# Optimization experiments

Measured on AMD Instinct MI355X. Metric: run time of the kernel, lower is better.

Reference implementation:

```python
import jax, jax.numpy as jnp
import numpy as np

HIDDEN = 1024
HEADS = 16
HEAD_DIM = HIDDEN // HEADS
SCALE = 1.0 / float(np.sqrt(HEAD_DIM))


def setup_inputs() -> dict:
    key = jax.random.key(0)
    k1, k2, k3, k4 = jax.random.split(key, 4)
    B, N, C = 4, 2048, HIDDEN
    x = jax.random.normal(k1, (B, N, C), dtype=jnp.float32)
    # nn.Linear(C, 3C, bias=False): y = x @ W_qkv where W_qkv is [C, 3C]
    w_qkv = jax.random.normal(k2, (C, 3 * C), dtype=jnp.float32) * (1.0 / np.sqrt(C))
    # nn.Linear(C, C) with bias
    w_out = jax.random.normal(k3, (C, C), dtype=jnp.float32) * (1.0 / np.sqrt(C))
    b_out = jax.random.normal(k4, (C,), dtype=jnp.float32) * 0.01
    return {"x": x, "w_qkv": w_qkv, "w_out": w_out, "b_out": b_out}


def reference(x, w_qkv, w_out, b_out):
    B, N, C = x.shape
    H, D = HEADS, HEAD_DIM
    qkv = jnp.einsum("bnc,cf->bnf", x, w_qkv)  # [B, N, 3C]
    qkv = qkv.reshape(B, N, 3, H, D).transpose(2, 0, 3, 1, 4)  # [3, B, H, N, D]
    q, k, v = qkv[0], qkv[1], qkv[2]
    attn = jnp.einsum("bhnd,bhmd->bhnm", q, k) * SCALE  # [B, H, N, N]
    attn = jax.nn.softmax(attn, axis=-1)
    # dropout is identity in eval mode
    out = jnp.einsum("bhnm,bhmd->bhnd", attn, v)  # [B, H, N, D]
    out = out.transpose(0, 2, 1, 3).reshape(B, N, C)
    return jnp.einsum("bnc,co->bno", out, w_out) + b_out
```

## Files before the change

### kernel.cpp

```cpp
#include <hip/hip_runtime.h>
#include <hip/hip_bf16.h>
#include <stdint.h>

#define SEQ   2048
#define NBH   64
#define DH    64
#define CH    1024
#define MTOT  8192
#define QSCALE 0.1803368801111204f

typedef __bf16 bf16_t;
typedef bf16_t bf16x8 __attribute__((ext_vector_type(8)));
typedef float  f32x4  __attribute__((ext_vector_type(4)));
typedef float  f32x16 __attribute__((ext_vector_type(16)));

__device__ __forceinline__ bf16_t to_bf16(float f) {
  uint32_t u = __builtin_bit_cast(uint32_t, f);
  uint16_t r = (uint16_t)((u + 0x7fffu + ((u >> 16) & 1u)) >> 16);
  return __builtin_bit_cast(bf16_t, r);
}

__device__ __forceinline__ void gload_lds16(const void* g, void* l) {
  __builtin_amdgcn_global_load_lds(
      (const __attribute__((address_space(1))) uint32_t*)g,
      (__attribute__((address_space(3))) uint32_t*)l, 16, 0, 0);
}

__device__ __forceinline__ f32x4 mfma_bf16(bf16x8 a, bf16x8 b, f32x4 c) {
  return __builtin_amdgcn_mfma_f32_16x16x32_bf16(a, b, c, 0, 0, 0);
}
__device__ __forceinline__ f32x16 mfma32_bf16(bf16x8 a, bf16x8 b, f32x16 c) {
  return __builtin_amdgcn_mfma_f32_32x32x16_bf16(a, b, c, 0, 0, 0);
}

__device__ __forceinline__ float exp2_fast(float x) {
#if __has_builtin(__builtin_amdgcn_exp2f)
  return __builtin_amdgcn_exp2f(x);
#else
  float r;
  asm("v_exp_f32 %0, %1\ns_nop 0" : "=v"(r) : "v"(x));
  return r;
#endif
}

__device__ __forceinline__ uint32_t cvt_pk_bf16(float lo, float hi) {
  uint32_t r;
  asm("v_cvt_pk_bf16_f32 %0, %1, %2" : "=v"(r) : "v"(lo), "v"(hi));
  return r;
}

__device__ __forceinline__ void permlane32_swap(uint32_t& a, uint32_t& b) {
  asm("s_nop 1\n\tv_permlane32_swap_b32 %0, %1\n\ts_nop 1" : "+v"(a), "+v"(b));
}


__global__ void cvt_f32_bf16(const float* __restrict__ in, bf16_t* __restrict__ out, int n) {
  int i = (blockIdx.x * 256 + threadIdx.x) * 4;
  const int stride = gridDim.x * 256 * 4;
  for (; i < n; i += stride) {
    const float4 f = *reinterpret_cast<const float4*>(in + i);
    bf16_t tmp[4] = {to_bf16(f.x), to_bf16(f.y), to_bf16(f.z), to_bf16(f.w)};
    *reinterpret_cast<uint2*>(out + i) = *reinterpret_cast<uint2*>(tmp);
  }
}

__global__ __launch_bounds__(256) void transpose_cvt(
    const float* __restrict__ W, bf16_t* __restrict__ WT, int Kd, int Nd) {
  __shared__ float t[64 * 65];
  const int n0 = blockIdx.x * 64, k0 = blockIdx.y * 64;
  const int tid = threadIdx.x;
#pragma unroll
  for (int rr = 0; rr < 16; ++rr) {
    const int idx = rr * 256 + tid;
    const int r = idx >> 6, c = idx & 63;
    t[r * 65 + c] = W[(size_t)(k0 + r) * Nd + n0 + c];
  }
  __syncthreads();
#pragma unroll
  for (int rr = 0; rr < 16; ++rr) {
    const int idx = rr * 256 + tid;
    const int nr = idx >> 6, kc = idx & 63;
    WT[(size_t)(n0 + nr) * Kd + k0 + kc] = to_bf16(t[kc * 65 + nr]);
  }
}


template <int EPI>
__global__ __launch_bounds__(256, 3) void gemm_bt(
    const bf16_t* __restrict__ A, const bf16_t* __restrict__ BT, int K, int nx,
    bf16_t* __restrict__ qb, bf16_t* __restrict__ kb, bf16_t* __restrict__ vb,
    const float* __restrict__ bias, float* __restrict__ out) {
  __shared__ __attribute__((aligned(16))) bf16_t lA[128 * 64];
  __shared__ __attribute__((aligned(16))) bf16_t lB[128 * 64];
  const int tid = threadIdx.x;
  const int lane = tid & 63;
  const int wv = tid >> 6;
  const int wm = wv >> 1, wn = wv & 1;

  const int nwg = gridDim.x;
  int bid = blockIdx.x;
  bid = (bid & 7) * (nwg >> 3) + (bid >> 3);
  const int m0 = (bid / nx) * 128, n0 = (bid % nx) * 128;

  const int l15 = lane & 15, l16 = lane >> 4;

  f32x4 acc[4][4] = {};

  const int srow = tid >> 3;
  const int sch = tid & 7;

  for (int kt = 0; kt < K; kt += 64) {
#pragma unroll
    for (int c = 0; c < 4; ++c) {
      const int row = c * 32 + srow;
      const int cs = sch ^ (row & 7);
      gload_lds16(A + (size_t)(m0 + row) * K + kt + cs * 8, &lA[c * 2048 + tid * 8]);
    }
#pragma unroll
    for (int c = 0; c < 4; ++c) {
      const int row = c * 32 + srow;
      const int cs = sch ^ (row & 7);
      gload_lds16(BT + (size_t)(n0 + row) * K + kt + cs * 8, &lB[c * 2048 + tid * 8]);
    }
    __syncthreads();
#pragma unroll
    for (int ks = 0; ks < 2; ++ks) {
      bf16x8 af[4], bfr[4];
#pragma unroll
      for (int i = 0; i < 4; ++i) {
        const int ar = wm * 64 + i * 16 + l15;
        const int cha = (ks * 4 + l16) ^ (ar & 7);
        af[i] = *reinterpret_cast<const bf16x8*>(&lA[ar * 64 + cha * 8]);
        const int br = wn * 64 + i * 16 + l15;
        const int chb = (ks * 4 + l16) ^ (br & 7);
        bfr[i] = *reinterpret_cast<const bf16x8*>(&lB[br * 64 + chb * 8]);
      }
#pragma unroll
      for (int i = 0; i < 4; ++i)
#pragma unroll
        for (int j = 0; j < 4; ++j)
          acc[i][j] = mfma_bf16(af[i], bfr[j], acc[i][j]);
    }
    __syncthreads();
  }

  if (EPI == 0) {
    const int f0 = n0 + wn * 64;
    const int three = f0 >> 10;
#pragma unroll
    for (int i = 0; i < 4; ++i) {
#pragma unroll
      for (int j = 0; j < 4; ++j) {
#pragma unroll
        for (int r = 0; r < 4; ++r) {
          const int m = m0 + wm * 64 + i * 16 + l16 * 4 + r;
          const int f = f0 + j * 16 + l15;
          const int h = (f >> 6) & 15, d = f & 63;
          const int bh = (m >> 11) * 16 + h;
          const int n = m & 2047;
          const float val = acc[i][j][r];
          if (three == 0)
            qb[((size_t)bh * SEQ + n) * DH + d] = to_bf16(val * QSCALE);
          else if (three == 1)
            kb[((size_t)bh * SEQ + n) * DH + d] = to_bf16(val);
          else
            vb[((size_t)bh * DH + d) * SEQ + n] = to_bf16(val);
        }
      }
    }
  } else {
#pragma unroll
    for (int j = 0; j < 4; ++j) {
      const int cc = n0 + wn * 64 + j * 16 + l15;
      const float bb = bias[cc];
#pragma unroll
      for (int i = 0; i < 4; ++i) {
#pragma unroll
        for (int r = 0; r < 4; ++r) {
          const int m = m0 + wm * 64 + i * 16 + l16 * 4 + r;
          out[(size_t)m * CH + cc] = acc[i][j][r] + bb;
        }
      }
    }
  }
}

__global__ __launch_bounds__(256, 4) void attn_fwd(
    const bf16_t* __restrict__ Q, const bf16_t* __restrict__ K,
    const bf16_t* __restrict__ V, bf16_t* __restrict__ O) {
  __shared__ __attribute__((aligned(16))) bf16_t lK[2][64 * 64];
  __shared__ __attribute__((aligned(16))) bf16_t lV[2][64 * 64];
  const int tid = threadIdx.x;
  const int lane = tid & 63;
  const int wv = tid >> 6;
  const int l31 = lane & 31, hi = lane >> 5;

  const int lin = blockIdx.x;
  const int bh = (lin & 7) * 8 + ((lin >> 3) & 7);
  const int qb = lin >> 6;
  const int q0w = qb * 128 + wv * 32;

  const bf16_t* Qb = Q + (size_t)bh * SEQ * DH;
  const bf16_t* Kb = K + (size_t)bh * SEQ * DH;
  const bf16_t* Vb = V + (size_t)bh * DH * SEQ;

  bf16x8 qf[4];
#pragma unroll
  for (int ks = 0; ks < 4; ++ks)
    qf[ks] = *reinterpret_cast<const bf16x8*>(
        Qb + (size_t)(q0w + l31) * DH + ks * 16 + hi * 8);

  f32x16 o0 = {}, o1 = {};
  float rs = 0.f;

  const int srow = tid >> 3;
  const int sch = tid & 7;

  auto stage = [&](int buf, int kt0) {
#pragma unroll
    for (int c = 0; c < 2; ++c) {
      const int row = c * 32 + srow;
      const int cs = sch ^ (row & 7);
      gload_lds16(Kb + (size_t)(kt0 + row) * DH + cs * 8, &lK[buf][c * 2048 + tid * 8]);
      gload_lds16(Vb + (size_t)row * SEQ + kt0 + cs * 8, &lV[buf][c * 2048 + tid * 8]);
    }
  };

  stage(0, 0);
  __syncthreads();
  int cur = 0;

  for (int t = 0; t < SEQ / 64; ++t) {
    if (t + 1 < SEQ / 64) stage(cur ^ 1, (t + 1) * 64);

    f32x16 s0 = {}, s1 = {};
    __builtin_amdgcn_s_setprio(1);
#pragma unroll
    for (int ks = 0; ks < 4; ++ks) {
      {
        const int row = l31;
        const int ch = (ks * 2 + hi) ^ (row & 7);
        const bf16x8 kf = *reinterpret_cast<const bf16x8*>(&lK[cur][row * 64 + ch * 8]);
        s0 = mfma32_bf16(kf, qf[ks], s0);
      }
      {
        const int row = 32 + l31;
        const int ch = (ks * 2 + hi) ^ (row & 7);
        const bf16x8 kf = *reinterpret_cast<const bf16x8*>(&lK[cur][row * 64 + ch * 8]);
        s1 = mfma32_bf16(kf, qf[ks], s1);
      }
    }
    __builtin_amdgcn_s_setprio(0);

#pragma unroll
    for (int j = 0; j < 16; ++j) { s0[j] = exp2_fast(s0[j]); rs += s0[j]; }
#pragma unroll
    for (int j = 0; j < 16; ++j) { s1[j] = exp2_fast(s1[j]); rs += s1[j]; }

    bf16x8 pa[4];
    {
      uint32_t a0 = cvt_pk_bf16(s0[0], s0[1]),   b0 = cvt_pk_bf16(s0[4], s0[5]);
      uint32_t a1 = cvt_pk_bf16(s0[2], s0[3]),   b1 = cvt_pk_bf16(s0[6], s0[7]);
      uint32_t a2 = cvt_pk_bf16(s0[8], s0[9]),   b2 = cvt_pk_bf16(s0[12], s0[13]);
      uint32_t a3 = cvt_pk_bf16(s0[10], s0[11]), b3 = cvt_pk_bf16(s0[14], s0[15]);
      permlane32_swap(a0, b0);
      permlane32_swap(a1, b1);
      permlane32_swap(a2, b2);
      permlane32_swap(a3, b3);
      union { uint32_t u[4]; bf16x8 v; } ua, ub, uc, ud;
      ua.u[0] = a0; ua.u[1] = a1; ua.u[2] = b0; ua.u[3] = b1; pa[0] = ua.v;
      ub.u[0] = a2; ub.u[1] = a3; ub.u[2] = b2; ub.u[3] = b3; pa[1] = ub.v;
      uint32_t c0 = cvt_pk_bf16(s1[0], s1[1]),   d0 = cvt_pk_bf16(s1[4], s1[5]);
      uint32_t c1 = cvt_pk_bf16(s1[2], s1[3]),   d1 = cvt_pk_bf16(s1[6], s1[7]);
      uint32_t c2 = cvt_pk_bf16(s1[8], s1[9]),   d2 = cvt_pk_bf16(s1[12], s1[13]);
      uint32_t c3 = cvt_pk_bf16(s1[10], s1[11]), d3 = cvt_pk_bf16(s1[14], s1[15]);
      permlane32_swap(c0, d0);
      permlane32_swap(c1, d1);
      permlane32_swap(c2, d2);
      permlane32_swap(c3, d3);
      uc.u[0] = c0; uc.u[1] = c1; uc.u[2] = d0; uc.u[3] = d1; pa[2] = uc.v;
      ud.u[0] = c2; ud.u[1] = c3; ud.u[2] = d2; ud.u[3] = d3; pa[3] = ud.v;
    }

    __builtin_amdgcn_s_setprio(1);
#pragma unroll
    for (int tt = 0; tt < 4; ++tt) {
      {
        const int row = l31;
        const int ch = (tt * 2 + hi) ^ (row & 7);
        const bf16x8 vf = *reinterpret_cast<const bf16x8*>(&lV[cur][row * 64 + ch * 8]);
        o0 = mfma32_bf16(pa[tt], vf, o0);
      }
      {
        const int row = 32 + l31;
        const int ch = (tt * 2 + hi) ^ (row & 7);
        const bf16x8 vf = *reinterpret_cast<const bf16x8*>(&lV[cur][row * 64 + ch * 8]);
        o1 = mfma32_bf16(pa[tt], vf, o1);
      }
    }
    __builtin_amdgcn_s_setprio(0);

    __syncthreads();
    cur ^= 1;
  }

  uint32_t ra = __builtin_bit_cast(uint32_t, rs), rb2 = ra;
  permlane32_swap(ra, rb2);
  const float tot = __builtin_bit_cast(float, ra) + __builtin_bit_cast(float, rb2);
  const float rinv = 1.0f / tot;

  const int b = bh >> 4, h = bh & 15;
#pragma unroll
  for (int r = 0; r < 16; ++r) {
    const int qr = (r & 3) + 8 * (r >> 2) + 4 * hi;
    const float inv = __shfl(rinv, qr, 64);
    const size_t grow = (size_t)(b * SEQ + q0w + qr) * CH + h * DH;
    O[grow + l31]      = to_bf16(o0[r] * inv);
    O[grow + 32 + l31] = to_bf16(o1[r] * inv);
  }
}


extern "C" void kernel_launch(void* const* d_in, const int* in_sizes, int n_in,
                              void* d_out, int out_size, void* d_ws, size_t ws_size,
                              hipStream_t stream) {
  const float* x     = (const float*)d_in[0];
  const float* w_qkv = (const float*)d_in[1];
  const float* w_out = (const float*)d_in[2];
  const float* b_out = (const float*)d_in[3];
  float* out = (float*)d_out;

  char* ws = (char*)d_ws;
  bf16_t* xb    = (bf16_t*)(ws);
  bf16_t* wqkvT = (bf16_t*)(ws + 16777216);
  bf16_t* woT   = (bf16_t*)(ws + 23068672);
  bf16_t* Qb    = (bf16_t*)(ws + 25165824);
  bf16_t* Kb    = (bf16_t*)(ws + 41943040);
  bf16_t* Vb    = (bf16_t*)(ws + 58720256);
  bf16_t* Ab    = xb;

  cvt_f32_bf16<<<2048, 256, 0, stream>>>(x, xb, MTOT * CH);
  transpose_cvt<<<dim3(3 * CH / 64, CH / 64), 256, 0, stream>>>(w_qkv, wqkvT, CH, 3 * CH);
  transpose_cvt<<<dim3(CH / 64, CH / 64), 256, 0, stream>>>(w_out, woT, CH, CH);

  gemm_bt<0><<<(3 * CH / 128) * (MTOT / 128), 256, 0, stream>>>(
      xb, wqkvT, CH, 3 * CH / 128, Qb, Kb, Vb, nullptr, nullptr);

  attn_fwd<<<1024, 256, 0, stream>>>(Qb, Kb, Vb, Ab);

  gemm_bt<1><<<(CH / 128) * (MTOT / 128), 256, 0, stream>>>(
      Ab, woT, CH, CH / 128, nullptr, nullptr, nullptr, b_out, out);
}
```

Baseline: 187.3 us.

## Compute softmax row sums via MFMA with ones, restructure attention tile loop

Replaces the per-thread VALU accumulation of softmax row sums with an extra MFMA against a ones vector, so the denominators come out in the same layout as the output accumulators and no cross-lane shuffle is needed at the end. The attention loop is unrolled by two with fixed LDS buffer offsets and precomputed swizzled read addresses. The exp/pack of the second half is interleaved with the PV MFMAs of the first half. The V epilogue in the QKV GEMM now writes packed 4-element bf16 vectors instead of scalar stores. This adds MFMA work (bf16-rounded P in the sum) in exchange for fewer VALU adds and less address arithmetic.

```diff
diff --git a/kernel.cpp b/kernel.cpp
--- a/kernel.cpp
+++ b/kernel.cpp
@@ -147,24 +147,39 @@
   if (EPI == 0) {
     const int f0 = n0 + wn * 64;
     const int three = f0 >> 10;
-#pragma unroll
-    for (int i = 0; i < 4; ++i) {
-#pragma unroll
-      for (int j = 0; j < 4; ++j) {
-#pragma unroll
-        for (int r = 0; r < 4; ++r) {
-          const int m = m0 + wm * 64 + i * 16 + l16 * 4 + r;
+    if (three < 2) {
+#pragma unroll
+      for (int i = 0; i < 4; ++i) {
+#pragma unroll
+        for (int j = 0; j < 4; ++j) {
+#pragma unroll
+          for (int r = 0; r < 4; ++r) {
+            const int m = m0 + wm * 64 + i * 16 + l16 * 4 + r;
+            const int f = f0 + j * 16 + l15;
+            const int h = (f >> 6) & 15, d = f & 63;
+            const int bh = (m >> 11) * 16 + h;
+            const int n = m & 2047;
+            const float val = acc[i][j][r];
+            if (three == 0)
+              qb[((size_t)bh * SEQ + n) * DH + d] = to_bf16(val * QSCALE);
+            else
+              kb[((size_t)bh * SEQ + n) * DH + d] = to_bf16(val);
+          }
+        }
+      }
+    } else {
+#pragma unroll
+      for (int i = 0; i < 4; ++i) {
+#pragma unroll
+        for (int j = 0; j < 4; ++j) {
+          const int m = m0 + wm * 64 + i * 16 + l16 * 4;
           const int f = f0 + j * 16 + l15;
           const int h = (f >> 6) & 15, d = f & 63;
           const int bh = (m >> 11) * 16 + h;
           const int n = m & 2047;
-          const float val = acc[i][j][r];
-          if (three == 0)
-            qb[((size_t)bh * SEQ + n) * DH + d] = to_bf16(val * QSCALE);
-          else if (three == 1)
-            kb[((size_t)bh * SEQ + n) * DH + d] = to_bf16(val);
-          else
-            vb[((size_t)bh * DH + d) * SEQ + n] = to_bf16(val);
+          const uint2 pk = make_uint2(cvt_pk_bf16(acc[i][j][0], acc[i][j][1]),
+                                      cvt_pk_bf16(acc[i][j][2], acc[i][j][3]));
+          *reinterpret_cast<uint2*>(&vb[((size_t)bh * DH + d) * SEQ + n]) = pk;
         }
       }
     }
@@ -188,8 +203,7 @@
 __global__ __launch_bounds__(256, 4) void attn_fwd(
     const bf16_t* __restrict__ Q, const bf16_t* __restrict__ K,
     const bf16_t* __restrict__ V, bf16_t* __restrict__ O) {
-  __shared__ __attribute__((aligned(16))) bf16_t lK[2][64 * 64];
-  __shared__ __attribute__((aligned(16))) bf16_t lV[2][64 * 64];
+  __shared__ __attribute__((aligned(16))) char lds[32768];
   const int tid = threadIdx.x;
   const int lane = tid & 63;
   const int wv = tid >> 6;
@@ -210,8 +224,21 @@
     qf[ks] = *reinterpret_cast<const bf16x8*>(
         Qb + (size_t)(q0w + l31) * DH + ks * 16 + hi * 8);
 
+  bf16x8 ones;
+#pragma unroll
+  for (int j = 0; j < 8; ++j) ones[j] = __builtin_bit_cast(bf16_t, (uint16_t)0x3F80);
+
   f32x16 o0 = {}, o1 = {};
-  float rs = 0.f;
+  f32x16 osum = {};
+
+  uint32_t raddr[2][4];
+#pragma unroll
+  for (int h = 0; h < 2; ++h) {
+    const int row = h * 32 + l31;
+#pragma unroll
+    for (int j = 0; j < 4; ++j)
+      raddr[h][j] = row * 128 + ((((j * 2 + hi) ^ (row & 7))) << 4);
+  }
 
   const int srow = tid >> 3;
   const int sch = tid & 7;
@@ -221,99 +248,98 @@
     for (int c = 0; c < 2; ++c) {
       const int row = c * 32 + srow;
       const int cs = sch ^ (row & 7);
-      gload_lds16(Kb + (size_t)(kt0 + row) * DH + cs * 8, &lK[buf][c * 2048 + tid * 8]);
-      gload_lds16(Vb + (size_t)row * SEQ + kt0 + cs * 8, &lV[buf][c * 2048 + tid * 8]);
+      gload_lds16(Kb + (size_t)(kt0 + row) * DH + cs * 8,
+                  lds + buf * 16384 + c * 4096 + tid * 16);
+      gload_lds16(Vb + (size_t)row * SEQ + kt0 + cs * 8,
+                  lds + buf * 16384 + 8192 + c * 4096 + tid * 16);
     }
   };
+
+#define ATT_TILE(KOFF, VOFF)                                                   \
+  {                                                                            \
+    f32x16 s0 = {}, s1 = {};                                                   \
+    __builtin_amdgcn_s_setprio(1);                                             \
+    _Pragma("unroll") for (int j = 0; j < 4; ++j) {                            \
+      const bf16x8 kf0 = *reinterpret_cast<const bf16x8*>(lds + raddr[0][j] + (KOFF)); \
+      s0 = mfma32_bf16(kf0, qf[j], s0);                                        \
+      const bf16x8 kf1 = *reinterpret_cast<const bf16x8*>(lds + raddr[1][j] + (KOFF)); \
+      s1 = mfma32_bf16(kf1, qf[j], s1);                                        \
+    }                                                                          \
+    __builtin_amdgcn_s_setprio(0);                                             \
+    _Pragma("unroll") for (int j = 0; j < 16; ++j) s0[j] = exp2_fast(s0[j]);   \
+    bf16x8 pa0, pa1;                                                           \
+    {                                                                          \
+      uint32_t a0 = cvt_pk_bf16(s0[0], s0[1]),   b0 = cvt_pk_bf16(s0[4], s0[5]);   \
+      uint32_t a1 = cvt_pk_bf16(s0[2], s0[3]),   b1 = cvt_pk_bf16(s0[6], s0[7]);   \
+      uint32_t a2 = cvt_pk_bf16(s0[8], s0[9]),   b2 = cvt_pk_bf16(s0[12], s0[13]); \
+      uint32_t a3 = cvt_pk_bf16(s0[10], s0[11]), b3 = cvt_pk_bf16(s0[14], s0[15]); \
+      permlane32_swap(a0, b0); permlane32_swap(a1, b1);                        \
+      permlane32_swap(a2, b2); permlane32_swap(a3, b3);                        \
+      union { uint32_t u[4]; bf16x8 v; } ua, ub;                               \
+      ua.u[0] = a0; ua.u[1] = a1; ua.u[2] = b0; ua.u[3] = b1; pa0 = ua.v;      \
+      ub.u[0] = a2; ub.u[1] = a3; ub.u[2] = b2; ub.u[3] = b3; pa1 = ub.v;      \
+    }                                                                          \
+    __builtin_amdgcn_s_setprio(1);                                             \
+    {                                                                          \
+      const bf16x8 vf00 = *reinterpret_cast<const bf16x8*>(lds + raddr[0][0] + (VOFF)); \
+      o0 = mfma32_bf16(pa0, vf00, o0);                                         \
+      const bf16x8 vf01 = *reinterpret_cast<const bf16x8*>(lds + raddr[1][0] + (VOFF)); \
+      o1 = mfma32_bf16(pa0, vf01, o1);                                         \
+      osum = mfma32_bf16(pa0, ones, osum);                                     \
+      const bf16x8 vf10 = *reinterpret_cast<const bf16x8*>(lds + raddr[0][1] + (VOFF)); \
+      o0 = mfma32_bf16(pa1, vf10, o0);                                         \
+      const bf16x8 vf11 = *reinterpret_cast<const bf16x8*>(lds + raddr[1][1] + (VOFF)); \
+      o1 = mfma32_bf16(pa1, vf11, o1);                                         \
+      osum = mfma32_bf16(pa1, ones, osum);                                     \
+    }                                                                          \
+    __builtin_amdgcn_s_setprio(0);                                             \
+    _Pragma("unroll") for (int j = 0; j < 16; ++j) s1[j] = exp2_fast(s1[j]);   \
+    bf16x8 pa2, pa3;                                                           \
+    {                                                                          \
+      uint32_t c0 = cvt_pk_bf16(s1[0], s1[1]),   d0 = cvt_pk_bf16(s1[4], s1[5]);   \
+      uint32_t c1 = cvt_pk_bf16(s1[2], s1[3]),   d1 = cvt_pk_bf16(s1[6], s1[7]);   \
+      uint32_t c2 = cvt_pk_bf16(s1[8], s1[9]),   d2 = cvt_pk_bf16(s1[12], s1[13]); \
+      uint32_t c3 = cvt_pk_bf16(s1[10], s1[11]), d3 = cvt_pk_bf16(s1[14], s1[15]); \
+      permlane32_swap(c0, d0); permlane32_swap(c1, d1);                        \
+      permlane32_swap(c2, d2); permlane32_swap(c3, d3);                        \
+      union { uint32_t u[4]; bf16x8 v; } uc, ud;                               \
+      uc.u[0] = c0; uc.u[1] = c1; uc.u[2] = d0; uc.u[3] = d1; pa2 = uc.v;      \
+      ud.u[0] = c2; ud.u[1] = c3; ud.u[2] = d2; ud.u[3] = d3; pa3 = ud.v;      \
+    }                                                                          \
+    __builtin_amdgcn_s_setprio(1);                                             \
+    {                                                                          \
+      const bf16x8 vf20 = *reinterpret_cast<const bf16x8*>(lds + raddr[0][2] + (VOFF)); \
+      o0 = mfma32_bf16(pa2, vf20, o0);                                         \
+      const bf16x8 vf21 = *reinterpret_cast<const bf16x8*>(lds + raddr[1][2] + (VOFF)); \
+      o1 = mfma32_bf16(pa2, vf21, o1);                                         \
+      osum = mfma32_bf16(pa2, ones, osum);                                     \
+      const bf16x8 vf30 = *reinterpret_cast<const bf16x8*>(lds + raddr[0][3] + (VOFF)); \
+      o0 = mfma32_bf16(pa3, vf30, o0);                                         \
+      const bf16x8 vf31 = *reinterpret_cast<const bf16x8*>(lds + raddr[1][3] + (VOFF)); \
+      o1 = mfma32_bf16(pa3, vf31, o1);                                         \
+      osum = mfma32_bf16(pa3, ones, osum);                                     \
+    }                                                                          \
+    __builtin_amdgcn_s_setprio(0);                                             \
+  }
 
   stage(0, 0);
   __syncthreads();
-  int cur = 0;
-
-  for (int t = 0; t < SEQ / 64; ++t) {
-    if (t + 1 < SEQ / 64) stage(cur ^ 1, (t + 1) * 64);
-
-    f32x16 s0 = {}, s1 = {};
-    __builtin_amdgcn_s_setprio(1);
-#pragma unroll
-    for (int ks = 0; ks < 4; ++ks) {
-      {
-        const int row = l31;
-        const int ch = (ks * 2 + hi) ^ (row & 7);
-        const bf16x8 kf = *reinterpret_cast<const bf16x8*>(&lK[cur][row * 64 + ch * 8]);
-        s0 = mfma32_bf16(kf, qf[ks], s0);
-      }
-      {
-        const int row = 32 + l31;
-        const int ch = (ks * 2 + hi) ^ (row & 7);
-        const bf16x8 kf = *reinterpret_cast<const bf16x8*>(&lK[cur][row * 64 + ch * 8]);
-        s1 = mfma32_bf16(kf, qf[ks], s1);
-      }
-    }
-    __builtin_amdgcn_s_setprio(0);
-
-#pragma unroll
-    for (int j = 0; j < 16; ++j) { s0[j] = exp2_fast(s0[j]); rs += s0[j]; }
-#pragma unroll
-    for (int j = 0; j < 16; ++j) { s1[j] = exp2_fast(s1[j]); rs += s1[j]; }
-
-    bf16x8 pa[4];
-    {
-      uint32_t a0 = cvt_pk_bf16(s0[0], s0[1]),   b0 = cvt_pk_bf16(s0[4], s0[5]);
-      uint32_t a1 = cvt_pk_bf16(s0[2], s0[3]),   b1 = cvt_pk_bf16(s0[6], s0[7]);
-      uint32_t a2 = cvt_pk_bf16(s0[8], s0[9]),   b2 = cvt_pk_bf16(s0[12], s0[13]);
-      uint32_t a3 = cvt_pk_bf16(s0[10], s0[11]), b3 = cvt_pk_bf16(s0[14], s0[15]);
-      permlane32_swap(a0, b0);
-      permlane32_swap(a1, b1);
-      permlane32_swap(a2, b2);
-      permlane32_swap(a3, b3);
-      union { uint32_t u[4]; bf16x8 v; } ua, ub, uc, ud;
-      ua.u[0] = a0; ua.u[1] = a1; ua.u[2] = b0; ua.u[3] = b1; pa[0] = ua.v;
-      ub.u[0] = a2; ub.u[1] = a3; ub.u[2] = b2; ub.u[3] = b3; pa[1] = ub.v;
-      uint32_t c0 = cvt_pk_bf16(s1[0], s1[1]),   d0 = cvt_pk_bf16(s1[4], s1[5]);
-      uint32_t c1 = cvt_pk_bf16(s1[2], s1[3]),   d1 = cvt_pk_bf16(s1[6], s1[7]);
-      uint32_t c2 = cvt_pk_bf16(s1[8], s1[9]),   d2 = cvt_pk_bf16(s1[12], s1[13]);
-      uint32_t c3 = cvt_pk_bf16(s1[10], s1[11]), d3 = cvt_pk_bf16(s1[14], s1[15]);
-      permlane32_swap(c0, d0);
-      permlane32_swap(c1, d1);
-      permlane32_swap(c2, d2);
-      permlane32_swap(c3, d3);
-      uc.u[0] = c0; uc.u[1] = c1; uc.u[2] = d0; uc.u[3] = d1; pa[2] = uc.v;
-      ud.u[0] = c2; ud.u[1] = c3; ud.u[2] = d2; ud.u[3] = d3; pa[3] = ud.v;
-    }
-
-    __builtin_amdgcn_s_setprio(1);
-#pragma unroll
-    for (int tt = 0; tt < 4; ++tt) {
-      {
-        const int row = l31;
-        const int ch = (tt * 2 + hi) ^ (row & 7);
-        const bf16x8 vf = *reinterpret_cast<const bf16x8*>(&lV[cur][row * 64 + ch * 8]);
-        o0 = mfma32_bf16(pa[tt], vf, o0);
-      }
-      {
-        const int row = 32 + l31;
-        const int ch = (tt * 2 + hi) ^ (row & 7);
-        const bf16x8 vf = *reinterpret_cast<const bf16x8*>(&lV[cur][row * 64 + ch * 8]);
-        o1 = mfma32_bf16(pa[tt], vf, o1);
-      }
-    }
-    __builtin_amdgcn_s_setprio(0);
-
+
+  for (int t = 0; t < SEQ / 64; t += 2) {
+    stage(1, (t + 1) * 64);
+    ATT_TILE(0, 8192)
     __syncthreads();
-    cur ^= 1;
-  }
-
-  uint32_t ra = __builtin_bit_cast(uint32_t, rs), rb2 = ra;
-  permlane32_swap(ra, rb2);
-  const float tot = __builtin_bit_cast(float, ra) + __builtin_bit_cast(float, rb2);
-  const float rinv = 1.0f / tot;
+    if (t + 2 < SEQ / 64) stage(0, (t + 2) * 64);
+    ATT_TILE(16384, 24576)
+    __syncthreads();
+  }
+#undef ATT_TILE
 
   const int b = bh >> 4, h = bh & 15;
 #pragma unroll
   for (int r = 0; r < 16; ++r) {
     const int qr = (r & 3) + 8 * (r >> 2) + 4 * hi;
-    const float inv = __shfl(rinv, qr, 64);
+    const float inv = 1.0f / osum[r];
     const size_t grow = (size_t)(b * SEQ + q0w + qr) * CH + h * DH;
     O[grow + l31]      = to_bf16(o0[r] * inv);
     O[grow + 32 + l31] = to_bf16(o1[r] * inv);
```

Result: faster. 178.8 us (-4.5%).

## Triple-buffer attention K/V tiles with one barrier and vectorize V-transpose stores

Applied to the files above, without the earlier changes.

The attention loop moves from a double-buffered scheme with a trailing __syncthreads to a three-slot ring. Two tiles are prefetched ahead, and a manual s_waitcnt vmcnt(4) plus a single s_barrier guards each iteration. LDS read offsets are precomputed once per thread, and occupancy is lowered from 4 to 3 blocks to make room for the extra buffers. Separately, the QKV GEMM epilogue now writes the transposed V layout as packed 4×bf16 (8-byte) stores instead of scalar 2-byte scattered stores, which cuts store instruction count and write traffic.

```diff
diff --git a/kernel.cpp b/kernel.cpp
--- a/kernel.cpp
+++ b/kernel.cpp
@@ -147,24 +147,39 @@
   if (EPI == 0) {
     const int f0 = n0 + wn * 64;
     const int three = f0 >> 10;
-#pragma unroll
-    for (int i = 0; i < 4; ++i) {
-#pragma unroll
-      for (int j = 0; j < 4; ++j) {
-#pragma unroll
-        for (int r = 0; r < 4; ++r) {
-          const int m = m0 + wm * 64 + i * 16 + l16 * 4 + r;
+    if (three < 2) {
+#pragma unroll
+      for (int i = 0; i < 4; ++i) {
+#pragma unroll
+        for (int j = 0; j < 4; ++j) {
+#pragma unroll
+          for (int r = 0; r < 4; ++r) {
+            const int m = m0 + wm * 64 + i * 16 + l16 * 4 + r;
+            const int f = f0 + j * 16 + l15;
+            const int h = (f >> 6) & 15, d = f & 63;
+            const int bh = (m >> 11) * 16 + h;
+            const int n = m & 2047;
+            const float val = acc[i][j][r];
+            if (three == 0)
+              qb[((size_t)bh * SEQ + n) * DH + d] = to_bf16(val * QSCALE);
+            else
+              kb[((size_t)bh * SEQ + n) * DH + d] = to_bf16(val);
+          }
+        }
+      }
+    } else {
+#pragma unroll
+      for (int i = 0; i < 4; ++i) {
+#pragma unroll
+        for (int j = 0; j < 4; ++j) {
+          const int m = m0 + wm * 64 + i * 16 + l16 * 4;
           const int f = f0 + j * 16 + l15;
           const int h = (f >> 6) & 15, d = f & 63;
           const int bh = (m >> 11) * 16 + h;
           const int n = m & 2047;
-          const float val = acc[i][j][r];
-          if (three == 0)
-            qb[((size_t)bh * SEQ + n) * DH + d] = to_bf16(val * QSCALE);
-          else if (three == 1)
-            kb[((size_t)bh * SEQ + n) * DH + d] = to_bf16(val);
-          else
-            vb[((size_t)bh * DH + d) * SEQ + n] = to_bf16(val);
+          const uint2 pk = make_uint2(cvt_pk_bf16(acc[i][j][0], acc[i][j][1]),
+                                      cvt_pk_bf16(acc[i][j][2], acc[i][j][3]));
+          *reinterpret_cast<uint2*>(&vb[((size_t)bh * DH + d) * SEQ + n]) = pk;
         }
       }
     }
@@ -185,11 +200,11 @@
   }
 }
 
-__global__ __launch_bounds__(256, 4) void attn_fwd(
+__global__ __launch_bounds__(256, 3) void attn_fwd(
     const bf16_t* __restrict__ Q, const bf16_t* __restrict__ K,
     const bf16_t* __restrict__ V, bf16_t* __restrict__ O) {
-  __shared__ __attribute__((aligned(16))) bf16_t lK[2][64 * 64];
-  __shared__ __attribute__((aligned(16))) bf16_t lV[2][64 * 64];
+  __shared__ __attribute__((aligned(16))) bf16_t lK[3][64 * 64];
+  __shared__ __attribute__((aligned(16))) bf16_t lV[3][64 * 64];
   const int tid = threadIdx.x;
   const int lane = tid & 63;
   const int wv = tid >> 6;
@@ -213,6 +228,15 @@
   f32x16 o0 = {}, o1 = {};
   float rs = 0.f;
 
+  uint32_t raddr[2][4];
+#pragma unroll
+  for (int h = 0; h < 2; ++h) {
+    const int row = h * 32 + l31;
+#pragma unroll
+    for (int j = 0; j < 4; ++j)
+      raddr[h][j] = row * 128 + ((((j * 2 + hi) ^ (row & 7))) << 4);
+  }
+
   const int srow = tid >> 3;
   const int sch = tid & 7;
 
@@ -221,34 +245,24 @@
     for (int c = 0; c < 2; ++c) {
       const int row = c * 32 + srow;
       const int cs = sch ^ (row & 7);
-      gload_lds16(Kb + (size_t)(kt0 + row) * DH + cs * 8, &lK[buf][c * 2048 + tid * 8]);
-      gload_lds16(Vb + (size_t)row * SEQ + kt0 + cs * 8, &lV[buf][c * 2048 + tid * 8]);
+      gload_lds16(Kb + (size_t)(kt0 + row) * DH + cs * 8,
+                  reinterpret_cast<char*>(&lK[buf][0]) + c * 4096 + tid * 16);
+      gload_lds16(Vb + (size_t)row * SEQ + kt0 + cs * 8,
+                  reinterpret_cast<char*>(&lV[buf][0]) + c * 4096 + tid * 16);
     }
   };
 
-  stage(0, 0);
-  __syncthreads();
-  int cur = 0;
-
-  for (int t = 0; t < SEQ / 64; ++t) {
-    if (t + 1 < SEQ / 64) stage(cur ^ 1, (t + 1) * 64);
-
+  auto tile = [&](int buf) {
+    const char* kb0 = reinterpret_cast<const char*>(&lK[buf][0]);
+    const char* vb0 = reinterpret_cast<const char*>(&lV[buf][0]);
     f32x16 s0 = {}, s1 = {};
     __builtin_amdgcn_s_setprio(1);
 #pragma unroll
     for (int ks = 0; ks < 4; ++ks) {
-      {
-        const int row = l31;
-        const int ch = (ks * 2 + hi) ^ (row & 7);
-        const bf16x8 kf = *reinterpret_cast<const bf16x8*>(&lK[cur][row * 64 + ch * 8]);
-        s0 = mfma32_bf16(kf, qf[ks], s0);
-      }
-      {
-        const int row = 32 + l31;
-        const int ch = (ks * 2 + hi) ^ (row & 7);
-        const bf16x8 kf = *reinterpret_cast<const bf16x8*>(&lK[cur][row * 64 + ch * 8]);
-        s1 = mfma32_bf16(kf, qf[ks], s1);
-      }
+      const bf16x8 kf0 = *reinterpret_cast<const bf16x8*>(kb0 + raddr[0][ks]);
+      s0 = mfma32_bf16(kf0, qf[ks], s0);
+      const bf16x8 kf1 = *reinterpret_cast<const bf16x8*>(kb0 + raddr[1][ks]);
+      s1 = mfma32_bf16(kf1, qf[ks], s1);
     }
     __builtin_amdgcn_s_setprio(0);
 
@@ -267,7 +281,7 @@
       permlane32_swap(a1, b1);
       permlane32_swap(a2, b2);
       permlane32_swap(a3, b3);
-      union { uint32_t u[4]; bf16x8 v; } ua, ub, uc, ud;
+      union { uint32_t u[4]; bf16x8 v; } ua, ub;
       ua.u[0] = a0; ua.u[1] = a1; ua.u[2] = b0; ua.u[3] = b1; pa[0] = ua.v;
       ub.u[0] = a2; ub.u[1] = a3; ub.u[2] = b2; ub.u[3] = b3; pa[1] = ub.v;
       uint32_t c0 = cvt_pk_bf16(s1[0], s1[1]),   d0 = cvt_pk_bf16(s1[4], s1[5]);
@@ -278,6 +292,7 @@
       permlane32_swap(c1, d1);
       permlane32_swap(c2, d2);
       permlane32_swap(c3, d3);
+      union { uint32_t u[4]; bf16x8 v; } uc, ud;
       uc.u[0] = c0; uc.u[1] = c1; uc.u[2] = d0; uc.u[3] = d1; pa[2] = uc.v;
       ud.u[0] = c2; ud.u[1] = c3; ud.u[2] = d2; ud.u[3] = d3; pa[3] = ud.v;
     }
@@ -285,24 +300,28 @@
     __builtin_amdgcn_s_setprio(1);
 #pragma unroll
     for (int tt = 0; tt < 4; ++tt) {
-      {
-        const int row = l31;
-        const int ch = (tt * 2 + hi) ^ (row & 7);
-        const bf16x8 vf = *reinterpret_cast<const bf16x8*>(&lV[cur][row * 64 + ch * 8]);
-        o0 = mfma32_bf16(pa[tt], vf, o0);
-      }
-      {
-        const int row = 32 + l31;
-        const int ch = (tt * 2 + hi) ^ (row & 7);
-        const bf16x8 vf = *reinterpret_cast<const bf16x8*>(&lV[cur][row * 64 + ch * 8]);
-        o1 = mfma32_bf16(pa[tt], vf, o1);
-      }
+      const bf16x8 vf0 = *reinterpret_cast<const bf16x8*>(vb0 + raddr[0][tt]);
+      o0 = mfma32_bf16(pa[tt], vf0, o0);
+      const bf16x8 vf1 = *reinterpret_cast<const bf16x8*>(vb0 + raddr[1][tt]);
+      o1 = mfma32_bf16(pa[tt], vf1, o1);
     }
     __builtin_amdgcn_s_setprio(0);
-
-    __syncthreads();
-    cur ^= 1;
-  }
+  };
+
+  stage(0, 0);
+  stage(1, 64);
+  int buf = 0;
+  for (int t = 0; t < SEQ / 64 - 1; ++t) {
+    asm volatile("s_waitcnt vmcnt(4)\n\ts_barrier" ::: "memory");
+    if (t + 2 < SEQ / 64) {
+      int nb = buf + 2; if (nb >= 3) nb -= 3;
+      stage(nb, (t + 2) * 64);
+    }
+    tile(buf);
+    if (++buf == 3) buf = 0;
+  }
+  asm volatile("s_waitcnt vmcnt(0)\n\ts_barrier" ::: "memory");
+  tile(buf);
 
   uint32_t ra = __builtin_bit_cast(uint32_t, rs), rb2 = ra;
   permlane32_swap(ra, rb2);
```

New measurement: 188.2 us. Within noise of the previous version (+0.5%).

## Use 256x256 double-buffered tiles for QKV GEMM with packed V stores

Applied to the files above, without the earlier changes.

Replaces the 128x128 QKV projection GEMM with a dedicated 512-thread kernel that computes 256x256 output tiles. It double-buffers LDS using async global-to-LDS loads and explicit vmcnt waits, and writes the transposed V output as packed 4-element bf16 stores. The aim is to raise operand reuse per LDS load, overlap global loads with MFMA work, and cut scattered 2-byte stores. In exchange the kernel uses 128 KB of LDS and more accumulator registers, which limits occupancy, and it launches only 384 workgroups. The attention LDS addressing is rewritten in byte offsets with no change in behaviour.

```diff
diff --git a/kernel.cpp b/kernel.cpp
--- a/kernel.cpp
+++ b/kernel.cpp
@@ -84,11 +84,119 @@
   }
 }
 
-
-template <int EPI>
-__global__ __launch_bounds__(256, 3) void gemm_bt(
+__global__ __launch_bounds__(512, 2) void gemm256_qkv(
+    const bf16_t* __restrict__ A, const bf16_t* __restrict__ BT,
+    bf16_t* __restrict__ qb, bf16_t* __restrict__ kb, bf16_t* __restrict__ vb) {
+  __shared__ __attribute__((aligned(16))) bf16_t lA[2][256 * 64];
+  __shared__ __attribute__((aligned(16))) bf16_t lB[2][256 * 64];
+  const int tid = threadIdx.x;
+  const int lane = tid & 63;
+  const int wv = tid >> 6;
+  const int wr = wv >> 2, wc = wv & 3;
+  const int l15 = lane & 15, l16 = lane >> 4;
+
+  const int nwg = gridDim.x;
+  int bid = blockIdx.x;
+  bid = (bid & 7) * (nwg >> 3) + (bid >> 3);
+  const int m0 = (bid / 12) * 256, n0 = (bid % 12) * 256;
+
+  f32x4 acc[8][4] = {};
+
+  const int srow = tid >> 3;
+  const int sch = tid & 7;
+
+  auto stage = [&](int buf, int kt) {
+#pragma unroll
+    for (int c = 0; c < 4; ++c) {
+      const int row = c * 64 + srow;
+      const int cs = sch ^ (row & 7);
+      gload_lds16(A + (size_t)(m0 + row) * CH + kt + cs * 8,
+                  reinterpret_cast<char*>(&lA[buf][0]) + c * 8192 + tid * 16);
+      gload_lds16(BT + (size_t)(n0 + row) * CH + kt + cs * 8,
+                  reinterpret_cast<char*>(&lB[buf][0]) + c * 8192 + tid * 16);
+    }
+  };
+
+  stage(0, 0);
+  stage(1, 64);
+
+  for (int t = 0; t < 16; ++t) {
+    if (t < 15)
+      asm volatile("s_waitcnt vmcnt(8)\n\ts_barrier" ::: "memory");
+    else
+      asm volatile("s_waitcnt vmcnt(0)\n\ts_barrier" ::: "memory");
+    const bf16_t* lap = &lA[t & 1][0];
+    const bf16_t* lbp = &lB[t & 1][0];
+
+    bf16x8 bfr[4][2];
+#pragma unroll
+    for (int j = 0; j < 4; ++j) {
+      const int br = wc * 64 + j * 16 + l15;
+#pragma unroll
+      for (int ks = 0; ks < 2; ++ks) {
+        const int ch = (ks * 4 + l16) ^ (br & 7);
+        bfr[j][ks] = *reinterpret_cast<const bf16x8*>(&lbp[br * 64 + ch * 8]);
+      }
+    }
+#pragma unroll
+    for (int i = 0; i < 8; ++i) {
+      const int ar = wr * 128 + i * 16 + l15;
+      const int ch0 = l16 ^ (ar & 7);
+      const bf16x8 af0 = *reinterpret_cast<const bf16x8*>(&lap[ar * 64 + ch0 * 8]);
+      const int ch1 = (4 + l16) ^ (ar & 7);
+      const bf16x8 af1 = *reinterpret_cast<const bf16x8*>(&lap[ar * 64 + ch1 * 8]);
+#pragma unroll
+      for (int j = 0; j < 4; ++j) {
+        acc[i][j] = mfma_bf16(af0, bfr[j][0], acc[i][j]);
+        acc[i][j] = mfma_bf16(af1, bfr[j][1], acc[i][j]);
+      }
+    }
+    asm volatile("s_barrier" ::: "memory");
+    if (t + 2 < 16) stage(t & 1, (t + 2) * 64);
+  }
+
+  const int f0 = n0 + wc * 64;
+  const int three = n0 >> 10;
+  if (three < 2) {
+#pragma unroll
+    for (int i = 0; i < 8; ++i) {
+#pragma unroll
+      for (int j = 0; j < 4; ++j) {
+#pragma unroll
+        for (int r = 0; r < 4; ++r) {
+          const int m = m0 + wr * 128 + i * 16 + l16 * 4 + r;
+          const int f = f0 + j * 16 + l15;
+          const int h = (f >> 6) & 15, d = f & 63;
+          const int bh = (m >> 11) * 16 + h;
+          const int n = m & 2047;
+          const float val = acc[i][j][r];
+          if (three == 0)
+            qb[((size_t)bh * SEQ + n) * DH + d] = to_bf16(val * QSCALE);
+          else
+            kb[((size_t)bh * SEQ + n) * DH + d] = to_bf16(val);
+        }
+      }
+    }
+  } else {
+#pragma unroll
+    for (int i = 0; i < 8; ++i) {
+#pragma unroll
+      for (int j = 0; j < 4; ++j) {
+        const int m = m0 + wr * 128 + i * 16 + l16 * 4;
+        const int f = f0 + j * 16 + l15;
+        const int h = (f >> 6) & 15, d = f & 63;
+        const int bh = (m >> 11) * 16 + h;
+        const int n = m & 2047;
+        const uint2 pk = make_uint2(cvt_pk_bf16(acc[i][j][0], acc[i][j][1]),
+                                    cvt_pk_bf16(acc[i][j][2], acc[i][j][3]));
+        *reinterpret_cast<uint2*>(&vb[((size_t)bh * DH + d) * SEQ + n]) = pk;
+      }
+    }
+  }
+}
+
+__global__ __launch_bounds__(256, 3) void gemm_out(
     const bf16_t* __restrict__ A, const bf16_t* __restrict__ BT, int K, int nx,
-    bf16_t* __restrict__ qb, bf16_t* __restrict__ kb, bf16_t* __restrict__ vb,
     const float* __restrict__ bias, float* __restrict__ out) {
   __shared__ __attribute__((aligned(16))) bf16_t lA[128 * 64];
   __shared__ __attribute__((aligned(16))) bf16_t lB[128 * 64];
@@ -144,42 +252,16 @@
     __syncthreads();
   }
 
-  if (EPI == 0) {
-    const int f0 = n0 + wn * 64;
-    const int three = f0 >> 10;
+#pragma unroll
+  for (int j = 0; j < 4; ++j) {
+    const int cc = n0 + wn * 64 + j * 16 + l15;
+    const float bb = bias[cc];
 #pragma unroll
     for (int i = 0; i < 4; ++i) {
 #pragma unroll
-      for (int j = 0; j < 4; ++j) {
-#pragma unroll
-        for (int r = 0; r < 4; ++r) {
-          const int m = m0 + wm * 64 + i * 16 + l16 * 4 + r;
-          const int f = f0 + j * 16 + l15;
-          const int h = (f >> 6) & 15, d = f & 63;
-          const int bh = (m >> 11) * 16 + h;
-          const int n = m & 2047;
-          const float val = acc[i][j][r];
-          if (three == 0)
-            qb[((size_t)bh * SEQ + n) * DH + d] = to_bf16(val * QSCALE);
-          else if (three == 1)
-            kb[((size_t)bh * SEQ + n) * DH + d] = to_bf16(val);
-          else
-            vb[((size_t)bh * DH + d) * SEQ + n] = to_bf16(val);
-        }
-      }
-    }
-  } else {
-#pragma unroll
-    for (int j = 0; j < 4; ++j) {
-      const int cc = n0 + wn * 64 + j * 16 + l15;
-      const float bb = bias[cc];
-#pragma unroll
-      for (int i = 0; i < 4; ++i) {
-#pragma unroll
-        for (int r = 0; r < 4; ++r) {
-          const int m = m0 + wm * 64 + i * 16 + l16 * 4 + r;
-          out[(size_t)m * CH + cc] = acc[i][j][r] + bb;
-        }
+      for (int r = 0; r < 4; ++r) {
+        const int m = m0 + wm * 64 + i * 16 + l16 * 4 + r;
+        out[(size_t)m * CH + cc] = acc[i][j][r] + bb;
       }
     }
   }
@@ -221,8 +303,10 @@
     for (int c = 0; c < 2; ++c) {
       const int row = c * 32 + srow;
       const int cs = sch ^ (row & 7);
-      gload_lds16(Kb + (size_t)(kt0 + row) * DH + cs * 8, &lK[buf][c * 2048 + tid * 8]);
-      gload_lds16(Vb + (size_t)row * SEQ + kt0 + cs * 8, &lV[buf][c * 2048 + tid * 8]);
+      gload_lds16(Kb + (size_t)(kt0 + row) * DH + cs * 8,
+                  reinterpret_cast<char*>(&lK[buf][0]) + c * 4096 + tid * 16);
+      gload_lds16(Vb + (size_t)row * SEQ + kt0 + cs * 8,
+                  reinterpret_cast<char*>(&lV[buf][0]) + c * 4096 + tid * 16);
     }
   };
 
@@ -240,13 +324,15 @@
       {
         const int row = l31;
         const int ch = (ks * 2 + hi) ^ (row & 7);
-        const bf16x8 kf = *reinterpret_cast<const bf16x8*>(&lK[cur][row * 64 + ch * 8]);
+        const bf16x8 kf = *reinterpret_cast<const bf16x8*>(
+            reinterpret_cast<const char*>(&lK[cur][0]) + row * 128 + ch * 16);
         s0 = mfma32_bf16(kf, qf[ks], s0);
       }
       {
         const int row = 32 + l31;
         const int ch = (ks * 2 + hi) ^ (row & 7);
-        const bf16x8 kf = *reinterpret_cast<const bf16x8*>(&lK[cur][row * 64 + ch * 8]);
+        const bf16x8 kf = *reinterpret_cast<const bf16x8*>(
+            reinterpret_cast<const char*>(&lK[cur][0]) + row * 128 + ch * 16);
         s1 = mfma32_bf16(kf, qf[ks], s1);
       }
     }
@@ -288,13 +374,15 @@
       {
         const int row = l31;
         const int ch = (tt * 2 + hi) ^ (row & 7);
-        const bf16x8 vf = *reinterpret_cast<const bf16x8*>(&lV[cur][row * 64 + ch * 8]);
+        const bf16x8 vf = *reinterpret_cast<const bf16x8*>(
+            reinterpret_cast<const char*>(&lV[cur][0]) + row * 128 + ch * 16);
         o0 = mfma32_bf16(pa[tt], vf, o0);
       }
       {
         const int row = 32 + l31;
         const int ch = (tt * 2 + hi) ^ (row & 7);
-        const bf16x8 vf = *reinterpret_cast<const bf16x8*>(&lV[cur][row * 64 + ch * 8]);
+        const bf16x8 vf = *reinterpret_cast<const bf16x8*>(
+            reinterpret_cast<const char*>(&lV[cur][0]) + row * 128 + ch * 16);
         o1 = mfma32_bf16(pa[tt], vf, o1);
       }
     }
@@ -343,11 +431,11 @@
   transpose_cvt<<<dim3(3 * CH / 64, CH / 64), 256, 0, stream>>>(w_qkv, wqkvT, CH, 3 * CH);
   transpose_cvt<<<dim3(CH / 64, CH / 64), 256, 0, stream>>>(w_out, woT, CH, CH);
 
-  gemm_bt<0><<<(3 * CH / 128) * (MTOT / 128), 256, 0, stream>>>(
-      xb, wqkvT, CH, 3 * CH / 128, Qb, Kb, Vb, nullptr, nullptr);
+  gemm256_qkv<<<(MTOT / 256) * (3 * CH / 256), 512, 0, stream>>>(
+      xb, wqkvT, Qb, Kb, Vb);
 
   attn_fwd<<<1024, 256, 0, stream>>>(Qb, Kb, Vb, Ab);
 
-  gemm_bt<1><<<(CH / 128) * (MTOT / 128), 256, 0, stream>>>(
-      Ab, woT, CH, CH / 128, nullptr, nullptr, nullptr, b_out, out);
-}
+  gemm_out<<<(CH / 128) * (MTOT / 128), 256, 0, stream>>>(
+      Ab, woT, CH, CH / 128, b_out, out);
+}
```

New measurement: 184.0 us. No clear change (-1.7%).
